# Kernel tuning notes

Measured on AMD Instinct MI355X. Metric: run time of the kernel, lower is better.

## Reference

```python
import jax, jax.numpy as jnp
import numpy as np
import math

B, S, D, H = 8, 1024, 1024, 16
HD = D // H  # head_features = 64
SCALE = math.sqrt(HD)


def setup_inputs() -> dict:
    key = jax.random.key(0)
    k0, k1, k2, k3, k4 = jax.random.split(key, 5)
    x = jax.random.normal(k0, (B, S, D), dtype=jnp.float32)
    attn_mask = (jax.random.uniform(k1, (B, S, S)) < 0.9).astype(jnp.float32)
    w_scale = 1.0 / math.sqrt(D)  # keep unsafe exp in finite range
    Wq = jax.random.normal(k2, (D, D), dtype=jnp.float32) * w_scale
    Wk = jax.random.normal(k3, (D, D), dtype=jnp.float32) * w_scale
    Wv = jax.random.normal(k4, (D, D), dtype=jnp.float32) * w_scale
    return {"x": x, "attn_mask": attn_mask, "Wq": Wq, "Wk": Wk, "Wv": Wv}


def reference(x, attn_mask, Wq, Wk, Wv):
    b, s, _ = x.shape

    def split_heads(t):  # [b,s,D] -> [b,H,s,HD]
        return t.reshape(b, s, H, HD).transpose(0, 2, 1, 3)

    q = split_heads(x @ Wq)
    k = split_heads(x @ Wk)
    v = split_heads(x @ Wv)

    # unsafe softmax: exp without max subtraction, multiplicative mask, +1e-8 denom
    scores = jnp.einsum('bhsd,bhtd->bhst', q, k) / SCALE
    e = jnp.exp(scores) * attn_mask[:, None, :, :]
    w = e / (e.sum(axis=3, keepdims=True) + 1e-8)

    ctx = jnp.einsum('bhst,bhtd->bhsd', w, v)  # [b,H,s,HD]
    return ctx.transpose(0, 2, 1, 3).reshape(b, s, D)
```

## Files before the change

kernel.cpp:

```cpp
#include <hip/hip_runtime.h>

#define KDIM 1024

typedef _Float16 half8 __attribute__((ext_vector_type(8)));
typedef _Float16 half4 __attribute__((ext_vector_type(4)));
typedef float f32x4 __attribute__((ext_vector_type(4)));

#if defined(__has_builtin)
#if __has_builtin(__builtin_amdgcn_global_load_lds)
#define HAVE_GLDS 1
#endif
#endif

__device__ __forceinline__ void stage16(const _Float16* g, _Float16* wave_base, int lane) {
#ifdef HAVE_GLDS
  __builtin_amdgcn_global_load_lds(
      (const __attribute__((address_space(1))) void*)g,
      (__attribute__((address_space(3))) void*)wave_base, 16, 0, 0);
#else
  *(half8*)(wave_base + lane * 8) = *(const half8*)g;
#endif
}

__global__ void cast_x_kernel(const float* __restrict__ x, _Float16* __restrict__ xb) {
  size_t i = ((size_t)blockIdx.x * 256 + threadIdx.x) * 4;
  float4 v = *(const float4*)(x + i);
  half4 h = { (_Float16)v.x, (_Float16)v.y, (_Float16)v.z, (_Float16)v.w };
  *(half4*)(xb + i) = h;
}

__global__ void wtrans_kernel(const float* __restrict__ Wq, const float* __restrict__ Wk,
                              const float* __restrict__ Wv, _Float16* __restrict__ Wqt,
                              _Float16* __restrict__ Wkt, _Float16* __restrict__ Wvt) {
  const float* src = blockIdx.z == 0 ? Wq : (blockIdx.z == 1 ? Wk : Wv);
  _Float16* dst = blockIdx.z == 0 ? Wqt : (blockIdx.z == 1 ? Wkt : Wvt);
  __shared__ _Float16 tile[32][33];
  int tx = threadIdx.x & 31, ty = threadIdx.x >> 5;
  int c0 = blockIdx.x * 32, r0 = blockIdx.y * 32;
#pragma unroll
  for (int i = 0; i < 4; i++) {
    int r = r0 + ty + i * 8;
    tile[tx][ty + i * 8] = (_Float16)src[(size_t)r * KDIM + c0 + tx];
  }
  __syncthreads();
#pragma unroll
  for (int i = 0; i < 4; i++) {
    int n = c0 + ty + i * 8;
    dst[(size_t)n * KDIM + r0 + tx] = tile[ty + i * 8][tx];
  }
}

__global__ void maskbits_kernel(const float* __restrict__ m, unsigned long long* __restrict__ bits) {
  size_t i = (size_t)blockIdx.x * 256 + threadIdx.x;
  unsigned long long b = __ballot(m[i] != 0.0f);
  if ((threadIdx.x & 63) == 0) bits[i >> 6] = b;
}

__global__ __launch_bounds__(256, 2)
void gemm_kernel(const _Float16* __restrict__ A, const _Float16* __restrict__ Bt,
                 _Float16* __restrict__ out, int mode, float scale) {
  __shared__ _Float16 As[128 * 32];
  __shared__ _Float16 Bs[128 * 32];
  int tid = threadIdx.x;
  int lane = tid & 63, w4 = tid >> 6;
  int la = lane & 15, qd = lane >> 4;
  int wm = w4 & 1, wn = w4 >> 1;
  int m0 = blockIdx.y * 128, n0 = blockIdx.x * 128;
  int r = tid >> 2, c = (tid & 3) * 8;
  const _Float16* Ag = A + (size_t)(m0 + r) * KDIM + c;
  const _Float16* Bg = Bt + (size_t)(n0 + r) * KDIM + c;
  _Float16* a0 = As + w4 * 512;
  _Float16* b0 = Bs + w4 * 512;
  f32x4 acc[4][4] = {};
  for (int kt = 0; kt < KDIM; kt += 32) {
    stage16(Ag + kt, a0, lane);
    stage16(Ag + (size_t)64 * KDIM + kt, a0 + 2048, lane);
    stage16(Bg + kt, b0, lane);
    stage16(Bg + (size_t)64 * KDIM + kt, b0 + 2048, lane);
    __syncthreads();
    half8 af[4], bf[4];
#pragma unroll
    for (int mi = 0; mi < 4; mi++)
      af[mi] = *(const half8*)(As + (wm * 64 + mi * 16 + la) * 32 + qd * 8);
#pragma unroll
    for (int ni = 0; ni < 4; ni++)
      bf[ni] = *(const half8*)(Bs + (wn * 64 + ni * 16 + la) * 32 + qd * 8);
#pragma unroll
    for (int mi = 0; mi < 4; mi++)
#pragma unroll
      for (int ni = 0; ni < 4; ni++)
        acc[mi][ni] = __builtin_amdgcn_mfma_f32_16x16x32_f16(af[mi], bf[ni], acc[mi][ni], 0, 0, 0);
    __syncthreads();
  }
#pragma unroll
  for (int mi = 0; mi < 4; mi++)
#pragma unroll
    for (int ni = 0; ni < 4; ni++) {
      f32x4 v = acc[mi][ni];
      int mb = m0 + wm * 64 + mi * 16 + qd * 4;
      int n = n0 + wn * 64 + ni * 16 + la;
#pragma unroll
      for (int rg = 0; rg < 4; rg++) {
        int m = mb + rg;
        _Float16 hv = (_Float16)(v[rg] * scale);
        size_t addr;
        if (mode == 0) {
          int b = m >> 10, s = m & 1023, hh = n >> 6, d = n & 63;
          addr = (((size_t)(b * 16 + hh)) * 1024 + s) * 64 + d;
        } else {
          int b = n >> 10, s = n & 1023, hh = m >> 6, d = m & 63;
          addr = (((size_t)(b * 16 + hh)) * 64 + d) * 1024 + s;
        }
        out[addr] = hv;
      }
    }
}

__global__ __launch_bounds__(256, 2)
void attn_kernel(const _Float16* __restrict__ Q, const _Float16* __restrict__ K,
                 const _Float16* __restrict__ Vt, const unsigned long long* __restrict__ mbits,
                 float* __restrict__ out) {
  __shared__ _Float16 Ks[2 * 64 * 32];
  __shared__ _Float16 Vs[2 * 64 * 32];
  __shared__ _Float16 Ps[4 * 2 * 16 * 32];
  int tid = threadIdx.x;
  int lane = tid & 63, w4 = tid >> 6;
  int la = lane & 15, qd = lane >> 4;
  int qt = blockIdx.x, h = blockIdx.y, b = blockIdx.z;
  const _Float16* Qp = Q + ((size_t)(b * 16 + h)) * 1024 * 64;
  const _Float16* Kp = K + ((size_t)(b * 16 + h)) * 1024 * 64;
  const _Float16* Vp = Vt + ((size_t)(b * 16 + h)) * 64 * 1024;
  int q0w = qt * 64 + w4 * 16;
  half8 qf[2];
  qf[0] = *(const half8*)(Qp + (size_t)(q0w + la) * 64 + qd * 8);
  qf[1] = *(const half8*)(Qp + (size_t)(q0w + la) * 64 + 32 + qd * 8);
  f32x4 acco[4] = {};
  float rs[4] = {0.f, 0.f, 0.f, 0.f};
  int r = tid >> 2, c = (tid & 3) * 8;
  _Float16* kbase = Ks + w4 * 512;
  _Float16* vbase = Vs + w4 * 512;
  const unsigned long long* mrow = mbits + (size_t)b * 1024 * 16;
  for (int tt = 0; tt < 16; tt++) {
    stage16(Kp + (size_t)(tt * 64 + r) * 64 + c, kbase, lane);
    stage16(Kp + (size_t)(tt * 64 + r) * 64 + 32 + c, kbase + 2048, lane);
    stage16(Vp + (size_t)r * 1024 + tt * 64 + c, vbase, lane);
    stage16(Vp + (size_t)r * 1024 + tt * 64 + 32 + c, vbase + 2048, lane);
    __syncthreads();
    f32x4 accs[4] = {};
#pragma unroll
    for (int tsub = 0; tsub < 4; tsub++) {
#pragma unroll
      for (int ks = 0; ks < 2; ks++) {
        half8 kf = *(const half8*)(Ks + ks * 2048 + (tsub * 16 + la) * 32 + qd * 8);
        accs[tsub] = __builtin_amdgcn_mfma_f32_16x16x32_f16(qf[ks], kf, accs[tsub], 0, 0, 0);
      }
    }
    unsigned long long mw[4];
#pragma unroll
    for (int rg = 0; rg < 4; rg++)
      mw[rg] = mrow[(size_t)(qt * 64 + w4 * 16 + qd * 4 + rg) * 16 + tt];
#pragma unroll
    for (int tsub = 0; tsub < 4; tsub++) {
      int ks = tsub >> 1;
      int t32 = (tsub & 1) * 16 + la;
      int shift = tsub * 16 + la;
#pragma unroll
      for (int rg = 0; rg < 4; rg++) {
        float e = ((mw[rg] >> shift) & 1ull) ? __expf(accs[tsub][rg]) : 0.0f;
        rs[rg] += e;
        Ps[w4 * 1024 + ks * 512 + (qd * 4 + rg) * 32 + t32] = (_Float16)e;
      }
    }
#pragma unroll
    for (int ks = 0; ks < 2; ks++) {
      half8 pf = *(const half8*)(Ps + w4 * 1024 + ks * 512 + la * 32 + qd * 8);
#pragma unroll
      for (int nsub = 0; nsub < 4; nsub++) {
        half8 vf = *(const half8*)(Vs + ks * 2048 + (nsub * 16 + la) * 32 + qd * 8);
        acco[nsub] = __builtin_amdgcn_mfma_f32_16x16x32_f16(pf, vf, acco[nsub], 0, 0, 0);
      }
    }
    __syncthreads();
  }
#pragma unroll
  for (int rg = 0; rg < 4; rg++) {
#pragma unroll
    for (int off = 1; off < 16; off <<= 1) rs[rg] += __shfl_xor(rs[rg], off);
  }
  float inv[4];
#pragma unroll
  for (int rg = 0; rg < 4; rg++) inv[rg] = 1.0f / (rs[rg] + 1e-8f);
  float* op = out + (size_t)b * 1024 * 1024 + (size_t)h * 64;
#pragma unroll
  for (int nsub = 0; nsub < 4; nsub++)
#pragma unroll
    for (int rg = 0; rg < 4; rg++) {
      int s = q0w + qd * 4 + rg;
      op[(size_t)s * 1024 + nsub * 16 + la] = acco[nsub][rg] * inv[rg];
    }
}

extern "C" void kernel_launch(void* const* d_in, const int* in_sizes, int n_in,
                              void* d_out, int out_size, void* d_ws, size_t ws_size,
                              hipStream_t stream) {
  (void)in_sizes; (void)n_in; (void)out_size; (void)ws_size;
  const float* x = (const float*)d_in[0];
  const float* am = (const float*)d_in[1];
  const float* Wq = (const float*)d_in[2];
  const float* Wk = (const float*)d_in[3];
  const float* Wv = (const float*)d_in[4];
  float* out = (float*)d_out;

  char* p = (char*)d_ws;
  _Float16* xb = (_Float16*)p;  p += (size_t)8192 * 1024 * 2;
  _Float16* Wqt = (_Float16*)p; p += (size_t)1024 * 1024 * 2;
  _Float16* Wkt = (_Float16*)p; p += (size_t)1024 * 1024 * 2;
  _Float16* Wvt = (_Float16*)p; p += (size_t)1024 * 1024 * 2;
  _Float16* Qh = (_Float16*)p;  p += (size_t)8192 * 1024 * 2;
  _Float16* Kh = (_Float16*)p;  p += (size_t)8192 * 1024 * 2;
  _Float16* Vth = (_Float16*)p; p += (size_t)8192 * 1024 * 2;
  unsigned long long* mb = (unsigned long long*)p;

  cast_x_kernel<<<8192, 256, 0, stream>>>(x, xb);
  wtrans_kernel<<<dim3(32, 32, 3), 256, 0, stream>>>(Wq, Wk, Wv, Wqt, Wkt, Wvt);
  maskbits_kernel<<<32768, 256, 0, stream>>>(am, mb);
  gemm_kernel<<<dim3(8, 64), 256, 0, stream>>>(xb, Wqt, Qh, 0, 0.125f);
  gemm_kernel<<<dim3(8, 64), 256, 0, stream>>>(xb, Wkt, Kh, 0, 1.0f);
  gemm_kernel<<<dim3(64, 8), 256, 0, stream>>>(Wvt, xb, Vth, 1, 1.0f);
  attn_kernel<<<dim3(16, 16, 8), 256, 0, stream>>>(Qh, Kh, Vth, mb, out);
}
```

Baseline: 282.3 us.

## Fuse QKV projections into one GEMM and keep attention probabilities in registers

Concatenates the three transposed weights, folding the Q scale into the weight cast, so one GEMM launch produces Q (transposed), K and V (transposed) with vectorized half4 stores for the transposed outputs. The attention kernel now computes S^T by swapping the MFMA operands, so exp'd probabilities land directly in the register layout needed for a 16x16x16 PV MFMA. This removes the LDS round-trip for P and halves the per-row sum shuffles. It also remaps block indices for locality and raises the occupancy hint to 4. Q is now loaded with strided scalar reads, and the PV step moves to narrower MFMAs.

```diff
diff --git a/kernel.cpp b/kernel.cpp
--- a/kernel.cpp
+++ b/kernel.cpp
@@ -30,17 +30,18 @@
 }
 
 __global__ void wtrans_kernel(const float* __restrict__ Wq, const float* __restrict__ Wk,
-                              const float* __restrict__ Wv, _Float16* __restrict__ Wqt,
-                              _Float16* __restrict__ Wkt, _Float16* __restrict__ Wvt) {
-  const float* src = blockIdx.z == 0 ? Wq : (blockIdx.z == 1 ? Wk : Wv);
-  _Float16* dst = blockIdx.z == 0 ? Wqt : (blockIdx.z == 1 ? Wkt : Wvt);
+                              const float* __restrict__ Wv, _Float16* __restrict__ Wqkvt) {
+  int z = blockIdx.z;
+  const float* src = z == 0 ? Wq : (z == 1 ? Wk : Wv);
+  _Float16* dst = Wqkvt + (size_t)z * KDIM * KDIM;
+  float sc = (z == 0) ? 0.125f : 1.0f;
   __shared__ _Float16 tile[32][33];
   int tx = threadIdx.x & 31, ty = threadIdx.x >> 5;
   int c0 = blockIdx.x * 32, r0 = blockIdx.y * 32;
 #pragma unroll
   for (int i = 0; i < 4; i++) {
     int r = r0 + ty + i * 8;
-    tile[tx][ty + i * 8] = (_Float16)src[(size_t)r * KDIM + c0 + tx];
+    tile[tx][ty + i * 8] = (_Float16)(src[(size_t)r * KDIM + c0 + tx] * sc);
   }
   __syncthreads();
 #pragma unroll
@@ -58,7 +59,8 @@
 
 __global__ __launch_bounds__(256, 2)
 void gemm_kernel(const _Float16* __restrict__ A, const _Float16* __restrict__ Bt,
-                 _Float16* __restrict__ out, int mode, float scale) {
+                 _Float16* __restrict__ Qt, _Float16* __restrict__ Kh,
+                 _Float16* __restrict__ Vth) {
   __shared__ _Float16 As[128 * 32];
   __shared__ _Float16 Bs[128 * 32];
   int tid = threadIdx.x;
@@ -92,50 +94,55 @@
         acc[mi][ni] = __builtin_amdgcn_mfma_f32_16x16x32_f16(af[mi], bf[ni], acc[mi][ni], 0, 0, 0);
     __syncthreads();
   }
+  int which = n0 >> 10;
+  int hh = ((n0 + wn * 64) >> 6) & 15;
 #pragma unroll
   for (int mi = 0; mi < 4; mi++)
 #pragma unroll
     for (int ni = 0; ni < 4; ni++) {
       f32x4 v = acc[mi][ni];
       int mb = m0 + wm * 64 + mi * 16 + qd * 4;
-      int n = n0 + wn * 64 + ni * 16 + la;
-#pragma unroll
-      for (int rg = 0; rg < 4; rg++) {
-        int m = mb + rg;
-        _Float16 hv = (_Float16)(v[rg] * scale);
-        size_t addr;
-        if (mode == 0) {
-          int b = m >> 10, s = m & 1023, hh = n >> 6, d = n & 63;
-          addr = (((size_t)(b * 16 + hh)) * 1024 + s) * 64 + d;
-        } else {
-          int b = n >> 10, s = n & 1023, hh = m >> 6, d = m & 63;
-          addr = (((size_t)(b * 16 + hh)) * 64 + d) * 1024 + s;
-        }
-        out[addr] = hv;
+      int b = mb >> 10, s = mb & 1023;
+      int d = ni * 16 + la;
+      if (which == 1) {
+#pragma unroll
+        for (int rg = 0; rg < 4; rg++)
+          Kh[(((size_t)(b * 16 + hh)) * 1024 + s + rg) * 64 + d] = (_Float16)v[rg];
+      } else {
+        _Float16* dst = (which == 0) ? Qt : Vth;
+        half4 h = { (_Float16)v[0], (_Float16)v[1], (_Float16)v[2], (_Float16)v[3] };
+        *(half4*)(dst + (((size_t)(b * 16 + hh)) * 64 + d) * 1024 + s) = h;
       }
     }
 }
 
-__global__ __launch_bounds__(256, 2)
-void attn_kernel(const _Float16* __restrict__ Q, const _Float16* __restrict__ K,
+__global__ __launch_bounds__(256, 4)
+void attn_kernel(const _Float16* __restrict__ Qt, const _Float16* __restrict__ K,
                  const _Float16* __restrict__ Vt, const unsigned long long* __restrict__ mbits,
                  float* __restrict__ out) {
   __shared__ _Float16 Ks[2 * 64 * 32];
   __shared__ _Float16 Vs[2 * 64 * 32];
-  __shared__ _Float16 Ps[4 * 2 * 16 * 32];
   int tid = threadIdx.x;
   int lane = tid & 63, w4 = tid >> 6;
   int la = lane & 15, qd = lane >> 4;
-  int qt = blockIdx.x, h = blockIdx.y, b = blockIdx.z;
-  const _Float16* Qp = Q + ((size_t)(b * 16 + h)) * 1024 * 64;
+  int linear = blockIdx.x;
+  int xlo = linear & 7;
+  int tmp = linear >> 3;
+  int qt = tmp & 15;
+  int hb = (tmp >> 4) * 8 + xlo;
+  int h = hb & 15, b = hb >> 4;
+  const _Float16* Qp = Qt + ((size_t)(b * 16 + h)) * 64 * 1024;
   const _Float16* Kp = K + ((size_t)(b * 16 + h)) * 1024 * 64;
   const _Float16* Vp = Vt + ((size_t)(b * 16 + h)) * 64 * 1024;
   int q0w = qt * 64 + w4 * 16;
   half8 qf[2];
-  qf[0] = *(const half8*)(Qp + (size_t)(q0w + la) * 64 + qd * 8);
-  qf[1] = *(const half8*)(Qp + (size_t)(q0w + la) * 64 + 32 + qd * 8);
+#pragma unroll
+  for (int ks = 0; ks < 2; ks++)
+#pragma unroll
+    for (int j = 0; j < 8; j++)
+      qf[ks][j] = Qp[(size_t)(ks * 32 + qd * 8 + j) * 1024 + q0w + la];
   f32x4 acco[4] = {};
-  float rs[4] = {0.f, 0.f, 0.f, 0.f};
+  float rs = 0.0f;
   int r = tid >> 2, c = (tid & 3) * 8;
   _Float16* kbase = Ks + w4 * 512;
   _Float16* vbase = Vs + w4 * 512;
@@ -148,56 +155,43 @@
     __syncthreads();
     f32x4 accs[4] = {};
 #pragma unroll
-    for (int tsub = 0; tsub < 4; tsub++) {
+    for (int tsub = 0; tsub < 4; tsub++)
 #pragma unroll
       for (int ks = 0; ks < 2; ks++) {
         half8 kf = *(const half8*)(Ks + ks * 2048 + (tsub * 16 + la) * 32 + qd * 8);
-        accs[tsub] = __builtin_amdgcn_mfma_f32_16x16x32_f16(qf[ks], kf, accs[tsub], 0, 0, 0);
+        accs[tsub] = __builtin_amdgcn_mfma_f32_16x16x32_f16(kf, qf[ks], accs[tsub], 0, 0, 0);
+      }
+    unsigned long long mw = mrow[(size_t)(q0w + la) * 16 + tt];
+#pragma unroll
+    for (int tsub = 0; tsub < 4; tsub++) {
+      half4 pf;
+#pragma unroll
+      for (int rg = 0; rg < 4; rg++) {
+        float e = ((mw >> (tsub * 16 + qd * 4 + rg)) & 1ull) ? __expf(accs[tsub][rg]) : 0.0f;
+        rs += e;
+        pf[rg] = (_Float16)e;
+      }
+#pragma unroll
+      for (int nsub = 0; nsub < 4; nsub++) {
+        half4 vf = *(const half4*)(Vs + (tsub >> 1) * 2048 + (nsub * 16 + la) * 32 +
+                                   (tsub & 1) * 16 + qd * 4);
+        acco[nsub] = __builtin_amdgcn_mfma_f32_16x16x16f16(pf, vf, acco[nsub], 0, 0, 0);
       }
     }
-    unsigned long long mw[4];
-#pragma unroll
-    for (int rg = 0; rg < 4; rg++)
-      mw[rg] = mrow[(size_t)(qt * 64 + w4 * 16 + qd * 4 + rg) * 16 + tt];
-#pragma unroll
-    for (int tsub = 0; tsub < 4; tsub++) {
-      int ks = tsub >> 1;
-      int t32 = (tsub & 1) * 16 + la;
-      int shift = tsub * 16 + la;
-#pragma unroll
-      for (int rg = 0; rg < 4; rg++) {
-        float e = ((mw[rg] >> shift) & 1ull) ? __expf(accs[tsub][rg]) : 0.0f;
-        rs[rg] += e;
-        Ps[w4 * 1024 + ks * 512 + (qd * 4 + rg) * 32 + t32] = (_Float16)e;
-      }
-    }
-#pragma unroll
-    for (int ks = 0; ks < 2; ks++) {
-      half8 pf = *(const half8*)(Ps + w4 * 1024 + ks * 512 + la * 32 + qd * 8);
-#pragma unroll
-      for (int nsub = 0; nsub < 4; nsub++) {
-        half8 vf = *(const half8*)(Vs + ks * 2048 + (nsub * 16 + la) * 32 + qd * 8);
-        acco[nsub] = __builtin_amdgcn_mfma_f32_16x16x32_f16(pf, vf, acco[nsub], 0, 0, 0);
-      }
-    }
-    __syncthreads();
-  }
+    __syncthreads();
+  }
+  rs += __shfl_xor(rs, 16);
+  rs += __shfl_xor(rs, 32);
+  float inv_q = 1.0f / (rs + 1e-8f);
+  float* op = out + (size_t)b * 1024 * 1024 + (size_t)h * 64;
 #pragma unroll
   for (int rg = 0; rg < 4; rg++) {
-#pragma unroll
-    for (int off = 1; off < 16; off <<= 1) rs[rg] += __shfl_xor(rs[rg], off);
-  }
-  float inv[4];
-#pragma unroll
-  for (int rg = 0; rg < 4; rg++) inv[rg] = 1.0f / (rs[rg] + 1e-8f);
-  float* op = out + (size_t)b * 1024 * 1024 + (size_t)h * 64;
-#pragma unroll
-  for (int nsub = 0; nsub < 4; nsub++)
-#pragma unroll
-    for (int rg = 0; rg < 4; rg++) {
-      int s = q0w + qd * 4 + rg;
-      op[(size_t)s * 1024 + nsub * 16 + la] = acco[nsub][rg] * inv[rg];
-    }
+    float inv = __shfl(inv_q, qd * 4 + rg);
+    int s = q0w + qd * 4 + rg;
+#pragma unroll
+    for (int nsub = 0; nsub < 4; nsub++)
+      op[(size_t)s * 1024 + nsub * 16 + la] = acco[nsub][rg] * inv;
+  }
 }
 
 extern "C" void kernel_launch(void* const* d_in, const int* in_sizes, int n_in,
@@ -212,20 +206,16 @@
   float* out = (float*)d_out;
 
   char* p = (char*)d_ws;
-  _Float16* xb = (_Float16*)p;  p += (size_t)8192 * 1024 * 2;
-  _Float16* Wqt = (_Float16*)p; p += (size_t)1024 * 1024 * 2;
-  _Float16* Wkt = (_Float16*)p; p += (size_t)1024 * 1024 * 2;
-  _Float16* Wvt = (_Float16*)p; p += (size_t)1024 * 1024 * 2;
-  _Float16* Qh = (_Float16*)p;  p += (size_t)8192 * 1024 * 2;
-  _Float16* Kh = (_Float16*)p;  p += (size_t)8192 * 1024 * 2;
-  _Float16* Vth = (_Float16*)p; p += (size_t)8192 * 1024 * 2;
+  _Float16* xb = (_Float16*)p;    p += (size_t)8192 * 1024 * 2;
+  _Float16* Wqkvt = (_Float16*)p; p += (size_t)3 * 1024 * 1024 * 2;
+  _Float16* Qt = (_Float16*)p;    p += (size_t)8192 * 1024 * 2;
+  _Float16* Kh = (_Float16*)p;    p += (size_t)8192 * 1024 * 2;
+  _Float16* Vth = (_Float16*)p;   p += (size_t)8192 * 1024 * 2;
   unsigned long long* mb = (unsigned long long*)p;
 
   cast_x_kernel<<<8192, 256, 0, stream>>>(x, xb);
-  wtrans_kernel<<<dim3(32, 32, 3), 256, 0, stream>>>(Wq, Wk, Wv, Wqt, Wkt, Wvt);
+  wtrans_kernel<<<dim3(32, 32, 3), 256, 0, stream>>>(Wq, Wk, Wv, Wqkvt);
   maskbits_kernel<<<32768, 256, 0, stream>>>(am, mb);
-  gemm_kernel<<<dim3(8, 64), 256, 0, stream>>>(xb, Wqt, Qh, 0, 0.125f);
-  gemm_kernel<<<dim3(8, 64), 256, 0, stream>>>(xb, Wkt, Kh, 0, 1.0f);
-  gemm_kernel<<<dim3(64, 8), 256, 0, stream>>>(Wvt, xb, Vth, 1, 1.0f);
-  attn_kernel<<<dim3(16, 16, 8), 256, 0, stream>>>(Qh, Kh, Vth, mb, out);
-}
+  gemm_kernel<<<dim3(24, 64), 256, 0, stream>>>(xb, Wqkvt, Qt, Kh, Vth);
+  attn_kernel<<<2048, 256, 0, stream>>>(Qt, Kh, Vth, mb, out);
+}
```

Result: slower. 328.3 us (+16.3%).
